# Kernel tuning notes

Hardware: AMD Instinct MI355X
Metric: run time of the kernel (lower is better)

## Reference

```python
import jax, jax.numpy as jnp
import numpy as np

B, S, H, NH = 4, 2048, 1024, 16
HD = H // NH  # 64


def setup_inputs() -> dict:
    key = jax.random.key(0)
    ks = jax.random.split(key, 9)
    s = 1.0 / np.sqrt(H)
    return {
        "hidden_state": jax.random.normal(ks[0], (B, S, H), dtype=jnp.float32),
        "Wq": jax.random.normal(ks[1], (H, H), dtype=jnp.float32) * s,
        "bq": jnp.zeros((H,), dtype=jnp.float32),
        "Wk": jax.random.normal(ks[2], (H, HD), dtype=jnp.float32) * s,
        "bk": jnp.zeros((HD,), dtype=jnp.float32),
        "Wv": jax.random.normal(ks[3], (H, HD), dtype=jnp.float32) * s,
        "bv": jnp.zeros((HD,), dtype=jnp.float32),
        "Wo": jax.random.normal(ks[4], (H, H), dtype=jnp.float32) * s,
        "bo": jnp.zeros((H,), dtype=jnp.float32),
    }


def reference(hidden_state, Wq, bq, Wk, bk, Wv, bv, Wo, bo):
    b, s = hidden_state.shape[0], hidden_state.shape[1]
    q = hidden_state @ Wq + bq                      # [B,S,H]
    k = hidden_state @ Wk + bk                      # [B,S,HD] (single shared KV head)
    v = hidden_state @ Wv + bv                      # [B,S,HD]
    q = q.reshape(b, s, NH, HD).transpose(0, 2, 1, 3)  # [B,NH,S,HD]
    scale = 1.0 / jnp.sqrt(jnp.float32(HD))
    # shared K head: broadcast over NH without materializing expanded K/V
    scores = jnp.einsum("bhqd,bkd->bhqk", q, k) * scale  # [B,NH,S,S]
    probs = jax.nn.softmax(scores, axis=-1)
    out = jnp.einsum("bhqk,bkd->bhqd", probs, v)         # [B,NH,S,HD]
    out = out.transpose(0, 2, 1, 3).reshape(b, s, NH * HD)
    return out @ Wo + bo
```

## Files before the change

### kernel.cpp

```cpp
#include <hip/hip_runtime.h>
#include <hip/hip_bf16.h>
#include <stdint.h>

#define B_ 4
#define S_ 2048
#define H_ 1024
#define NH_ 16
#define HD_ 64

typedef __bf16 bf16x8 __attribute__((ext_vector_type(8)));
typedef float floatx4 __attribute__((ext_vector_type(4)));

__device__ __forceinline__ float b2f(unsigned short u) {
  union { float f; unsigned int i; } x; x.i = ((unsigned int)u) << 16; return x.f;
}
__device__ __forceinline__ unsigned short f2b(float f) {
  unsigned int u = __float_as_uint(f);
  u += 0x7fff + ((u >> 16) & 1);
  return (unsigned short)(u >> 16);
}

__device__ __forceinline__ void gload_lds16(const unsigned short* g, unsigned short* l) {
  __builtin_amdgcn_global_load_lds(
      (const __attribute__((address_space(1))) unsigned int*)(uintptr_t)g,
      (__attribute__((address_space(3))) unsigned int*)(uintptr_t)l,
      16, 0, 0);
}


__global__ __launch_bounds__(256) void convert_f32_bf16(
    const float* __restrict__ s, unsigned short* __restrict__ d, int n) {
  int i0 = (blockIdx.x * 256 + threadIdx.x) * 8;
  if (i0 >= n) return;
  float4 a = *(const float4*)(s + i0);
  float4 b = *(const float4*)(s + i0 + 4);
  union { unsigned short u[8]; uint4 v; } p;
  p.u[0] = f2b(a.x); p.u[1] = f2b(a.y); p.u[2] = f2b(a.z); p.u[3] = f2b(a.w);
  p.u[4] = f2b(b.x); p.u[5] = f2b(b.y); p.u[6] = f2b(b.z); p.u[7] = f2b(b.w);
  *(uint4*)(d + i0) = p.v;
}

__global__ __launch_bounds__(256) void transpose_f32_bf16(
    const float* __restrict__ src, unsigned short* __restrict__ dst,
    int R, int C) {
  __shared__ unsigned short tile[64][65];
  const int c0 = blockIdx.x * 64;
  const int r0 = blockIdx.y * 64;
  const int tx = threadIdx.x;
  const int ty = threadIdx.y;
  for (int i = ty; i < 64; i += 4)
    tile[i][tx] = f2b(src[(size_t)(r0 + i) * C + c0 + tx]);
  __syncthreads();
  for (int i = ty; i < 64; i += 4)
    dst[(size_t)(c0 + i) * R + r0 + tx] = tile[tx][i];
}

__global__ void build_kvbias(const float* __restrict__ bk,
                             const float* __restrict__ bv,
                             float* __restrict__ kvb) {
  int i = threadIdx.x;
  kvb[i] = (i < 64) ? bk[i] : bv[i - 64];
}

__global__ __launch_bounds__(256) void vtrans(const unsigned short* __restrict__ KV,
                                              unsigned short* __restrict__ Vt) {
  int idx = blockIdx.x * 256 + threadIdx.x;
  int s = idx & (S_ - 1);
  int d = (idx >> 11) & 63;
  int b = idx >> 17;
  Vt[idx] = KV[((size_t)(b * S_ + s)) * 128 + 64 + d];
}


__global__ __launch_bounds__(256) void gemm_qkv(
    const unsigned short* __restrict__ A,
    const unsigned short* __restrict__ Bt,
    const float* __restrict__ bq,
    const float* __restrict__ kvb,
    unsigned short* __restrict__ Qm,
    unsigned short* __restrict__ KVm,
    int M, int K) {
  __shared__ unsigned short As[4096];
  __shared__ unsigned short Bs[4096];
  const int m0 = blockIdx.x * 128;
  const int n0 = blockIdx.y * 128;
  const int t = threadIdx.x;
  const int lane = t & 63;
  const int w = t >> 6;
  const int wr = (w & 1) * 64;
  const int wc = (w >> 1) * 64;
  const int lrow = lane & 15;
  const int lk = (lane >> 4) * 8;

  floatx4 acc[4][4] = {};

  const unsigned short* Ap = A + (size_t)(m0 + (t >> 2)) * K + (t & 3) * 8;
  const unsigned short* Bp = Bt + (size_t)(n0 + (t >> 2)) * K + (t & 3) * 8;
  const size_t rowstep = (size_t)64 * K;

  for (int k0 = 0; k0 < K; k0 += 32) {
    __syncthreads();
    gload_lds16(Ap + k0,           &As[w * 512]);
    gload_lds16(Ap + k0 + rowstep, &As[2048 + w * 512]);
    gload_lds16(Bp + k0,           &Bs[w * 512]);
    gload_lds16(Bp + k0 + rowstep, &Bs[2048 + w * 512]);
    __syncthreads();
    bf16x8 a[4], b[4];
#pragma unroll
    for (int i = 0; i < 4; i++)
      a[i] = *(const bf16x8*)&As[(wr + i * 16 + lrow) * 32 + lk];
#pragma unroll
    for (int j = 0; j < 4; j++)
      b[j] = *(const bf16x8*)&Bs[(wc + j * 16 + lrow) * 32 + lk];
#pragma unroll
    for (int i = 0; i < 4; i++)
#pragma unroll
      for (int j = 0; j < 4; j++)
        acc[i][j] = __builtin_amdgcn_mfma_f32_16x16x32_bf16(a[i], b[j], acc[i][j], 0, 0, 0);
  }
  const bool isQ = (n0 < 1024);
#pragma unroll
  for (int j = 0; j < 4; j++) {
    int col = n0 + wc + j * 16 + lrow;
    float bj = isQ ? bq[col] : kvb[col - 1024];
#pragma unroll
    for (int i = 0; i < 4; i++) {
      int row0 = m0 + wr + i * 16 + (lane >> 4) * 4;
#pragma unroll
      for (int r = 0; r < 4; r++) {
        unsigned short v = f2b(acc[i][j][r] + bj);
        if (isQ) Qm[(size_t)(row0 + r) * 1024 + col] = v;
        else     KVm[(size_t)(row0 + r) * 128 + col - 1024] = v;
      }
    }
  }
}


__global__ __launch_bounds__(256) void gemm_out(
    const unsigned short* __restrict__ A,
    const unsigned short* __restrict__ Bt,
    const float* __restrict__ bias,
    float* __restrict__ C,
    int M, int N, int K) {
  __shared__ unsigned short As[4096];
  __shared__ unsigned short Bs[4096];
  const int m0 = blockIdx.x * 128;
  const int n0 = blockIdx.y * 128;
  const int t = threadIdx.x;
  const int lane = t & 63;
  const int w = t >> 6;
  const int wr = (w & 1) * 64;
  const int wc = (w >> 1) * 64;
  const int lrow = lane & 15;
  const int lk = (lane >> 4) * 8;

  floatx4 acc[4][4] = {};

  const unsigned short* Ap = A + (size_t)(m0 + (t >> 2)) * K + (t & 3) * 8;
  const unsigned short* Bp = Bt + (size_t)(n0 + (t >> 2)) * K + (t & 3) * 8;
  const size_t rowstep = (size_t)64 * K;

  for (int k0 = 0; k0 < K; k0 += 32) {
    __syncthreads();
    gload_lds16(Ap + k0,           &As[w * 512]);
    gload_lds16(Ap + k0 + rowstep, &As[2048 + w * 512]);
    gload_lds16(Bp + k0,           &Bs[w * 512]);
    gload_lds16(Bp + k0 + rowstep, &Bs[2048 + w * 512]);
    __syncthreads();
    bf16x8 a[4], b[4];
#pragma unroll
    for (int i = 0; i < 4; i++)
      a[i] = *(const bf16x8*)&As[(wr + i * 16 + lrow) * 32 + lk];
#pragma unroll
    for (int j = 0; j < 4; j++)
      b[j] = *(const bf16x8*)&Bs[(wc + j * 16 + lrow) * 32 + lk];
#pragma unroll
    for (int i = 0; i < 4; i++)
#pragma unroll
      for (int j = 0; j < 4; j++)
        acc[i][j] = __builtin_amdgcn_mfma_f32_16x16x32_bf16(a[i], b[j], acc[i][j], 0, 0, 0);
  }
#pragma unroll
  for (int j = 0; j < 4; j++) {
    int col = n0 + wc + j * 16 + lrow;
    float bj = bias[col];
#pragma unroll
    for (int i = 0; i < 4; i++) {
      int row0 = m0 + wr + i * 16 + (lane >> 4) * 4;
#pragma unroll
      for (int r = 0; r < 4; r++)
        C[(size_t)(row0 + r) * N + col] = acc[i][j][r] + bj;
    }
  }
}


__global__ __launch_bounds__(256) void mqa_flash(
    const unsigned short* __restrict__ Q,
    const unsigned short* __restrict__ KV,
    const unsigned short* __restrict__ Vt,
    unsigned short* __restrict__ O) {
  __shared__ unsigned short Qs[4096];
  __shared__ unsigned short Ks[4096];
  __shared__ unsigned short Vs[4096];
  __shared__ __bf16 Ps[4][1024];

  const int bid = blockIdx.x;
  const int qb = bid & 31;
  const int h = (bid >> 5) & 15;
  const int b = bid >> 9;
  const int t = threadIdx.x;
  const int lane = t & 63;
  const int w = t >> 6;
  const int lrow = lane & 15;
  const int lk = (lane >> 4) * 8;

  const float scale2 = 0.125f * 1.44269504088896340736f;
  const float CAP = 10.0f;

  {
    const size_t qoff = (size_t)(b * S_ + qb * 64 + (t >> 2)) * H_ + h * HD_ + (t & 3) * 8;
    gload_lds16(Q + qoff,      &Qs[w * 512]);
    gload_lds16(Q + qoff + 32, &Qs[2048 + w * 512]);
  }
  __syncthreads();
  const bf16x8 qf0 = *(const bf16x8*)&Qs[(w * 16 + lrow) * 32 + lk];
  const bf16x8 qf1 = *(const bf16x8*)&Qs[2048 + (w * 16 + lrow) * 32 + lk];

  bf16x8 ones;
#pragma unroll
  for (int j = 0; j < 8; j++) ones[j] = (__bf16)1.0f;

  floatx4 oacc[4] = {};
  floatx4 lacc = {};

  const unsigned short* kp = KV + (size_t)(b * S_ + (t >> 2)) * 128 + (t & 3) * 8;
  const unsigned short* vp = Vt + (size_t)(b * 64 + (t >> 2)) * S_ + (t & 3) * 8;

  for (int kb = 0; kb < 32; kb++) {
    __syncthreads();
    gload_lds16(kp,      &Ks[w * 512]);
    gload_lds16(kp + 32, &Ks[2048 + w * 512]);
    gload_lds16(vp,      &Vs[w * 512]);
    gload_lds16(vp + 32, &Vs[2048 + w * 512]);
    kp += 64 * 128;
    vp += 64;
    __syncthreads();

    floatx4 sacc[4] = {};
#pragma unroll
    for (int kt = 0; kt < 4; kt++) {
      bf16x8 kf0 = *(const bf16x8*)&Ks[(kt * 16 + lrow) * 32 + lk];
      bf16x8 kf1 = *(const bf16x8*)&Ks[2048 + (kt * 16 + lrow) * 32 + lk];
      sacc[kt] = __builtin_amdgcn_mfma_f32_16x16x32_bf16(qf0, kf0, sacc[kt], 0, 0, 0);
      sacc[kt] = __builtin_amdgcn_mfma_f32_16x16x32_bf16(qf1, kf1, sacc[kt], 0, 0, 0);
    }

#pragma unroll
    for (int kt = 0; kt < 4; kt++) {
#pragma unroll
      for (int r = 0; r < 4; r++) {
        float p = exp2f(fmaf(sacc[kt][r], scale2, -CAP));
        Ps[w][(kt >> 1) * 512 + ((lane >> 4) * 4 + r) * 32 + lrow + (kt & 1) * 16] = (__bf16)p;
      }
    }
    asm volatile("" ::: "memory");

    bf16x8 pf0 = *(const bf16x8*)&Ps[w][lrow * 32 + lk];
    bf16x8 pf1 = *(const bf16x8*)&Ps[w][512 + lrow * 32 + lk];
#pragma unroll
    for (int j = 0; j < 4; j++) {
      bf16x8 vf0 = *(const bf16x8*)&Vs[(j * 16 + lrow) * 32 + lk];
      bf16x8 vf1 = *(const bf16x8*)&Vs[2048 + (j * 16 + lrow) * 32 + lk];
      oacc[j] = __builtin_amdgcn_mfma_f32_16x16x32_bf16(pf0, vf0, oacc[j], 0, 0, 0);
      oacc[j] = __builtin_amdgcn_mfma_f32_16x16x32_bf16(pf1, vf1, oacc[j], 0, 0, 0);
    }
    lacc = __builtin_amdgcn_mfma_f32_16x16x32_bf16(pf0, ones, lacc, 0, 0, 0);
    lacc = __builtin_amdgcn_mfma_f32_16x16x32_bf16(pf1, ones, lacc, 0, 0, 0);
  }

  float inv[4];
#pragma unroll
  for (int r = 0; r < 4; r++) inv[r] = 1.0f / lacc[r];
  const int row0 = b * S_ + qb * 64 + w * 16 + (lane >> 4) * 4;
#pragma unroll
  for (int j = 0; j < 4; j++) {
    int col = h * HD_ + j * 16 + lrow;
#pragma unroll
    for (int r = 0; r < 4; r++)
      O[(size_t)(row0 + r) * H_ + col] = f2b(oacc[j][r] * inv[r]);
  }
}


extern "C" void kernel_launch(void* const* d_in, const int* in_sizes, int n_in,
                              void* d_out, int out_size, void* d_ws, size_t ws_size,
                              hipStream_t stream) {
  const float* X  = (const float*)d_in[0];
  const float* Wq = (const float*)d_in[1];
  const float* bq = (const float*)d_in[2];
  const float* Wk = (const float*)d_in[3];
  const float* bk = (const float*)d_in[4];
  const float* Wv = (const float*)d_in[5];
  const float* bv = (const float*)d_in[6];
  const float* Wo = (const float*)d_in[7];
  const float* bo = (const float*)d_in[8];
  float* out = (float*)d_out;

  if (ws_size < 40108544) return;
  char* wsb = (char*)d_ws;
  unsigned short* Xc    = (unsigned short*)(wsb);
  unsigned short* WqkvT = (unsigned short*)(wsb + 16777216);
  unsigned short* WoT   = (unsigned short*)(wsb + 19136512);
  float*          kvb   = (float*)(wsb + 21233664);
  unsigned short* Qm    = (unsigned short*)(wsb + 21234176);
  unsigned short* KVm   = (unsigned short*)(wsb + 38011392);
  unsigned short* Om    = Xc;
  unsigned short* Vtm   = WqkvT;

  convert_f32_bf16<<<4096, 256, 0, stream>>>(X, Xc, 8192 * 1024);

  dim3 tb(64, 4);
  transpose_f32_bf16<<<dim3(16, 16), tb, 0, stream>>>(Wq, WqkvT, 1024, 1024);
  transpose_f32_bf16<<<dim3(1, 16),  tb, 0, stream>>>(Wk, WqkvT + (size_t)1024 * 1024, 1024, 64);
  transpose_f32_bf16<<<dim3(1, 16),  tb, 0, stream>>>(Wv, WqkvT + (size_t)1088 * 1024, 1024, 64);
  transpose_f32_bf16<<<dim3(16, 16), tb, 0, stream>>>(Wo, WoT, 1024, 1024);
  build_kvbias<<<1, 128, 0, stream>>>(bk, bv, kvb);

  gemm_qkv<<<dim3(64, 9), 256, 0, stream>>>(Xc, WqkvT, bq, kvb, Qm, KVm, 8192, 1024);
  vtrans<<<2048, 256, 0, stream>>>(KVm, Vtm);
  mqa_flash<<<2048, 256, 0, stream>>>(Qm, KVm, Vtm, Om);
  gemm_out<<<dim3(64, 8), 256, 0, stream>>>(Om, WoT, bo, out, 8192, 1024, 1024);
}
```

Measured before the change: 324.7 us.

## Rewrite MQA attention with 32x32 MFMA and pre-swizzled K/V fragment layouts

Replaces the 256-thread LDS-staged flash kernel with a single-wave kernel. It reads K and V fragments directly from global memory in a pre-swizzled MFMA operand layout built by new kf_build/vf_build kernels, double-buffers K in registers, and uses 32x32x16 MFMAs. P is passed between half-waves with shuffles instead of LDS, and the row sum is accumulated in scalar registers. This removes the block-wide syncs and LDS round trips, at the cost of higher register pressure, redundant K/V loads for each 32-query block, and two extra layout kernels.

Measured after the change: 346.6 us. 6.7% more time.

```diff
diff --git a/kernel.cpp b/kernel.cpp
--- a/kernel.cpp
+++ b/kernel.cpp
@@ -10,6 +10,7 @@
 
 typedef __bf16 bf16x8 __attribute__((ext_vector_type(8)));
 typedef float floatx4 __attribute__((ext_vector_type(4)));
+typedef float floatx16 __attribute__((ext_vector_type(16)));
 
 __device__ __forceinline__ float b2f(unsigned short u) {
   union { float f; unsigned int i; } x; x.i = ((unsigned int)u) << 16; return x.f;
@@ -62,13 +63,27 @@
   kvb[i] = (i < 64) ? bk[i] : bv[i - 64];
 }
 
-__global__ __launch_bounds__(256) void vtrans(const unsigned short* __restrict__ KV,
-                                              unsigned short* __restrict__ Vt) {
-  int idx = blockIdx.x * 256 + threadIdx.x;
-  int s = idx & (S_ - 1);
-  int d = (idx >> 11) & 63;
-  int b = idx >> 17;
-  Vt[idx] = KV[((size_t)(b * S_ + s)) * 128 + 64 + d];
+__global__ __launch_bounds__(256) void kf_build(const unsigned short* __restrict__ KVm,
+                                                unsigned short* __restrict__ KF) {
+  int tid = blockIdx.x * 256 + threadIdx.x;
+  int L = tid & 63, u = tid >> 6;
+  int cq = u & 3, kt = (u >> 2) & 1, kb = (u >> 3) & 31, b = u >> 8;
+  int row = b * 2048 + kb * 64 + kt * 32 + (L & 31);
+  int col = cq * 16 + (L >> 5) * 8;
+  *(uint4*)(KF + (size_t)tid * 8) = *(const uint4*)(KVm + (size_t)row * 128 + col);
+}
+
+__global__ __launch_bounds__(256) void vf_build(const unsigned short* __restrict__ KVm,
+                                                unsigned short* __restrict__ VF) {
+  int tid = blockIdx.x * 256 + threadIdx.x;
+  int L = tid & 63, u = tid >> 6;
+  int dt = u & 1, kh = (u >> 1) & 1, kt = (u >> 2) & 1, kb = (u >> 3) & 31, b = u >> 8;
+  int krow0 = b * 2048 + kb * 64 + kt * 32 + kh * 16 + (L >> 5) * 8;
+  int d = dt * 32 + (L & 31);
+  union { unsigned short t[8]; uint4 v; } tmp;
+#pragma unroll
+  for (int j = 0; j < 8; j++) tmp.t[j] = KVm[(size_t)(krow0 + j) * 128 + 64 + d];
+  *(uint4*)(VF + (size_t)tid * 8) = tmp.v;
 }
 
 
@@ -196,100 +211,116 @@
 }
 
 
-__global__ __launch_bounds__(256) void mqa_flash(
-    const unsigned short* __restrict__ Q,
-    const unsigned short* __restrict__ KV,
-    const unsigned short* __restrict__ Vt,
+__global__ __launch_bounds__(64) void mqa_flash2(
+    const unsigned short* __restrict__ Qm,
+    const unsigned short* __restrict__ KF,
+    const unsigned short* __restrict__ VF,
     unsigned short* __restrict__ O) {
-  __shared__ unsigned short Qs[4096];
-  __shared__ unsigned short Ks[4096];
-  __shared__ unsigned short Vs[4096];
-  __shared__ __bf16 Ps[4][1024];
+  __shared__ unsigned short T[32 * 72];
 
   const int bid = blockIdx.x;
-  const int qb = bid & 31;
-  const int h = (bid >> 5) & 15;
-  const int b = bid >> 9;
-  const int t = threadIdx.x;
-  const int lane = t & 63;
-  const int w = t >> 6;
-  const int lrow = lane & 15;
-  const int lk = (lane >> 4) * 8;
+  const int q32 = bid & 63;
+  const int h = (bid >> 6) & 15;
+  const int b = bid >> 10;
+  const int L = threadIdx.x;
+  const int q = L & 31;
+  const int hw = L >> 5;
 
   const float scale2 = 0.125f * 1.44269504088896340736f;
   const float CAP = 10.0f;
 
-  {
-    const size_t qoff = (size_t)(b * S_ + qb * 64 + (t >> 2)) * H_ + h * HD_ + (t & 3) * 8;
-    gload_lds16(Q + qoff,      &Qs[w * 512]);
-    gload_lds16(Q + qoff + 32, &Qs[2048 + w * 512]);
-  }
-  __syncthreads();
-  const bf16x8 qf0 = *(const bf16x8*)&Qs[(w * 16 + lrow) * 32 + lk];
-  const bf16x8 qf1 = *(const bf16x8*)&Qs[2048 + (w * 16 + lrow) * 32 + lk];
-
-  bf16x8 ones;
-#pragma unroll
-  for (int j = 0; j < 8; j++) ones[j] = (__bf16)1.0f;
-
-  floatx4 oacc[4] = {};
-  floatx4 lacc = {};
-
-  const unsigned short* kp = KV + (size_t)(b * S_ + (t >> 2)) * 128 + (t & 3) * 8;
-  const unsigned short* vp = Vt + (size_t)(b * 64 + (t >> 2)) * S_ + (t & 3) * 8;
+  const int qrow = b * S_ + q32 * 32 + q;
+  bf16x8 qf[4];
+#pragma unroll
+  for (int cq = 0; cq < 4; cq++)
+    qf[cq] = *(const bf16x8*)(Qm + (size_t)qrow * 1024 + h * 64 + cq * 16 + hw * 8);
+
+  floatx16 oacc[2] = {};
+  float l = 0.f;
+
+  const unsigned short* kfp = KF + (size_t)b * 131072 + L * 8;
+  const unsigned short* vfp = VF + (size_t)b * 131072 + L * 8;
+
+  bf16x8 kA[8], kB[8];
+#pragma unroll
+  for (int u = 0; u < 8; u++) kA[u] = *(const bf16x8*)(kfp + u * 512);
 
   for (int kb = 0; kb < 32; kb++) {
-    __syncthreads();
-    gload_lds16(kp,      &Ks[w * 512]);
-    gload_lds16(kp + 32, &Ks[2048 + w * 512]);
-    gload_lds16(vp,      &Vs[w * 512]);
-    gload_lds16(vp + 32, &Vs[2048 + w * 512]);
-    kp += 64 * 128;
-    vp += 64;
-    __syncthreads();
-
-    floatx4 sacc[4] = {};
-#pragma unroll
-    for (int kt = 0; kt < 4; kt++) {
-      bf16x8 kf0 = *(const bf16x8*)&Ks[(kt * 16 + lrow) * 32 + lk];
-      bf16x8 kf1 = *(const bf16x8*)&Ks[2048 + (kt * 16 + lrow) * 32 + lk];
-      sacc[kt] = __builtin_amdgcn_mfma_f32_16x16x32_bf16(qf0, kf0, sacc[kt], 0, 0, 0);
-      sacc[kt] = __builtin_amdgcn_mfma_f32_16x16x32_bf16(qf1, kf1, sacc[kt], 0, 0, 0);
+    bf16x8 vr[8];
+    const unsigned short* vp = vfp + (size_t)kb * 4096;
+#pragma unroll
+    for (int u = 0; u < 8; u++) vr[u] = *(const bf16x8*)(vp + u * 512);
+
+    const bf16x8* kcur = (kb & 1) ? kB : kA;
+    bf16x8* knxt = (kb & 1) ? kA : kB;
+
+    floatx16 sacc[2] = {};
+#pragma unroll
+    for (int kt = 0; kt < 2; kt++)
+#pragma unroll
+      for (int cq = 0; cq < 4; cq++)
+        sacc[kt] = __builtin_amdgcn_mfma_f32_32x32x16_bf16(kcur[kt * 4 + cq], qf[cq], sacc[kt], 0, 0, 0);
+
+    {
+      const unsigned short* kp = kfp + (size_t)(kb + 1) * 4096;
+#pragma unroll
+      for (int u = 0; u < 8; u++) knxt[u] = *(const bf16x8*)(kp + u * 512);
     }
 
-#pragma unroll
-    for (int kt = 0; kt < 4; kt++) {
-#pragma unroll
-      for (int r = 0; r < 4; r++) {
-        float p = exp2f(fmaf(sacc[kt][r], scale2, -CAP));
-        Ps[w][(kt >> 1) * 512 + ((lane >> 4) * 4 + r) * 32 + lrow + (kt & 1) * 16] = (__bf16)p;
+    unsigned int pk[2][8];
+#pragma unroll
+    for (int kt = 0; kt < 2; kt++)
+#pragma unroll
+      for (int i2 = 0; i2 < 8; i2++) {
+        float p0 = exp2f(fmaf(sacc[kt][2 * i2],     scale2, -CAP));
+        float p1 = exp2f(fmaf(sacc[kt][2 * i2 + 1], scale2, -CAP));
+        l += p0 + p1;
+        union { __bf16 h2[2]; unsigned int u; } pu;
+        pu.h2[0] = (__bf16)p0; pu.h2[1] = (__bf16)p1;
+        pk[kt][i2] = pu.u;
       }
+
+#pragma unroll
+    for (int kt = 0; kt < 2; kt++)
+#pragma unroll
+      for (int kh = 0; kh < 2; kh++) {
+        unsigned int s0 = hw ? pk[kt][kh * 4 + 0] : pk[kt][kh * 4 + 2];
+        unsigned int s1 = hw ? pk[kt][kh * 4 + 1] : pk[kt][kh * 4 + 3];
+        unsigned int r0 = (unsigned int)__shfl_xor((int)s0, 32, 64);
+        unsigned int r1 = (unsigned int)__shfl_xor((int)s1, 32, 64);
+        union { unsigned int u[4]; bf16x8 v; } fu;
+        if (hw == 0) {
+          fu.u[0] = pk[kt][kh * 4 + 0]; fu.u[1] = pk[kt][kh * 4 + 1];
+          fu.u[2] = r0;                 fu.u[3] = r1;
+        } else {
+          fu.u[0] = r0;                 fu.u[1] = r1;
+          fu.u[2] = pk[kt][kh * 4 + 2]; fu.u[3] = pk[kt][kh * 4 + 3];
+        }
+#pragma unroll
+        for (int dt = 0; dt < 2; dt++)
+          oacc[dt] = __builtin_amdgcn_mfma_f32_32x32x16_bf16(vr[kt * 4 + kh * 2 + dt], fu.v, oacc[dt], 0, 0, 0);
+      }
+  }
+
+  l += __shfl_xor(l, 32, 64);
+  float inv = 1.0f / l;
+#pragma unroll
+  for (int dt = 0; dt < 2; dt++)
+#pragma unroll
+    for (int g = 0; g < 4; g++) {
+      int d = dt * 32 + g * 8 + hw * 4;
+      union { __bf16 h4[4]; uint2 u; } ou;
+#pragma unroll
+      for (int r = 0; r < 4; r++) ou.h4[r] = (__bf16)(oacc[dt][g * 4 + r] * inv);
+      *(uint2*)&T[q * 72 + d] = ou.u;
     }
-    asm volatile("" ::: "memory");
-
-    bf16x8 pf0 = *(const bf16x8*)&Ps[w][lrow * 32 + lk];
-    bf16x8 pf1 = *(const bf16x8*)&Ps[w][512 + lrow * 32 + lk];
-#pragma unroll
-    for (int j = 0; j < 4; j++) {
-      bf16x8 vf0 = *(const bf16x8*)&Vs[(j * 16 + lrow) * 32 + lk];
-      bf16x8 vf1 = *(const bf16x8*)&Vs[2048 + (j * 16 + lrow) * 32 + lk];
-      oacc[j] = __builtin_amdgcn_mfma_f32_16x16x32_bf16(pf0, vf0, oacc[j], 0, 0, 0);
-      oacc[j] = __builtin_amdgcn_mfma_f32_16x16x32_bf16(pf1, vf1, oacc[j], 0, 0, 0);
-    }
-    lacc = __builtin_amdgcn_mfma_f32_16x16x32_bf16(pf0, ones, lacc, 0, 0, 0);
-    lacc = __builtin_amdgcn_mfma_f32_16x16x32_bf16(pf1, ones, lacc, 0, 0, 0);
-  }
-
-  float inv[4];
-#pragma unroll
-  for (int r = 0; r < 4; r++) inv[r] = 1.0f / lacc[r];
-  const int row0 = b * S_ + qb * 64 + w * 16 + (lane >> 4) * 4;
-#pragma unroll
-  for (int j = 0; j < 4; j++) {
-    int col = h * HD_ + j * 16 + lrow;
-#pragma unroll
-    for (int r = 0; r < 4; r++)
-      O[(size_t)(row0 + r) * H_ + col] = f2b(oacc[j][r] * inv[r]);
+  asm volatile("" ::: "memory");
+  int q2 = L >> 1, dh = (L & 1) * 32;
+  const size_t obase = ((size_t)(b * S_ + q32 * 32 + q2)) * 1024 + h * 64 + dh;
+#pragma unroll
+  for (int c = 0; c < 4; c++) {
+    uint4 vv = *(const uint4*)&T[q2 * 72 + dh + c * 8];
+    *(uint4*)(O + obase + c * 8) = vv;
   }
 }
 
@@ -317,7 +348,8 @@
   unsigned short* Qm    = (unsigned short*)(wsb + 21234176);
   unsigned short* KVm   = (unsigned short*)(wsb + 38011392);
   unsigned short* Om    = Xc;
-  unsigned short* Vtm   = WqkvT;
+  unsigned short* KF    = WqkvT;
+  unsigned short* VF    = WqkvT + (size_t)524288;
 
   convert_f32_bf16<<<4096, 256, 0, stream>>>(X, Xc, 8192 * 1024);
 
@@ -329,7 +361,8 @@
   build_kvbias<<<1, 128, 0, stream>>>(bk, bv, kvb);
 
   gemm_qkv<<<dim3(64, 9), 256, 0, stream>>>(Xc, WqkvT, bq, kvb, Qm, KVm, 8192, 1024);
-  vtrans<<<2048, 256, 0, stream>>>(KVm, Vtm);
-  mqa_flash<<<2048, 256, 0, stream>>>(Qm, KVm, Vtm, Om);
+  kf_build<<<256, 256, 0, stream>>>(KVm, KF);
+  vf_build<<<256, 256, 0, stream>>>(KVm, VF);
+  mqa_flash2<<<4096, 64, 0, stream>>>(Qm, KF, VF, Om);
   gemm_out<<<dim3(64, 8), 256, 0, stream>>>(Om, WoT, bo, out, 8192, 1024, 1024);
 }
```
